# Kernel optimization log

Hardware: AMD Instinct MI355X
Metric: run time of the kernel (lower is better)

The kernel has to match this reference:

```python
import jax, jax.numpy as jnp
import numpy as np

EPS = 1e-5

def conv1x1(x, W, b):
    # x: [B,C,H,W], W: [O,C], b: [O]
    return jnp.einsum('bchw,oc->bohw', x, W) + b[None, :, None, None]

def bn_eval(x, gamma, beta, mean, var):
    inv = jax.lax.rsqrt(var + EPS)
    return (x - mean[None, :, None, None]) * (gamma * inv)[None, :, None, None] + beta[None, :, None, None]

def setup_inputs() -> dict:
    key = jax.random.key(0)
    ks = jax.random.split(key, 12)
    B, C, O = 32, 256, 256
    Hz, Wz, Hx, Wx = 7, 7, 31, 31
    s = 0.02
    inp = {
        'zf': jax.random.normal(ks[0], (B, C, Hz, Wz), jnp.float32),
        'xf': jax.random.normal(ks[1], (B, C, Hx, Wx), jnp.float32),
        'Wq': jax.random.normal(ks[2], (C, C), jnp.float32) * s,
        'bq': jnp.zeros((C,), jnp.float32),
        'Ws': jax.random.normal(ks[3], (C, C), jnp.float32) * s,
        'bs': jnp.zeros((C,), jnp.float32),
        'Wg': jax.random.normal(ks[4], (C, C), jnp.float32) * s,
        'bg': jnp.zeros((C,), jnp.float32),
        'g_gamma': jnp.ones((C,), jnp.float32),
        'g_beta': jnp.zeros((C,), jnp.float32),
        'g_mean': jnp.zeros((C,), jnp.float32),
        'g_var': jnp.ones((C,), jnp.float32),
        'Wfi': jax.random.normal(ks[5], (O, 3 * C), jnp.float32) * s,
        'bfi': jnp.zeros((O,), jnp.float32),
        'fi_gamma': jnp.ones((O,), jnp.float32),
        'fi_beta': jnp.zeros((O,), jnp.float32),
        'fi_mean': jnp.zeros((O,), jnp.float32),
        'fi_var': jnp.ones((O,), jnp.float32),
    }
    return inp

def reference(zf, xf, Wq, bq, Ws, bs, Wg, bg, g_gamma, g_beta, g_mean, g_var,
              Wfi, bfi, fi_gamma, fi_beta, fi_mean, fi_var):
    B, C, Hx, Wx = xf.shape
    _, _, Hz, Wz = zf.shape
    Nx, Nz = Hx * Wx, Hz * Wz

    xf_trans = conv1x1(xf, Wq, bq)                 # [B,C,Hx,Wx]
    zf_trans = conv1x1(zf, Ws, bs)                 # [B,C,Hz,Wz]
    xf_g = jax.nn.relu(bn_eval(conv1x1(xf, Wg, bg), g_gamma, g_beta, g_mean, g_var))
    zf_g = jax.nn.relu(bn_eval(conv1x1(zf, Wg, bg), g_gamma, g_beta, g_mean, g_var))

    zf_g_p = zf_g.reshape(B, C, Nz).transpose(0, 2, 1)      # [B,Nz,C]
    xf_g_p = xf_g.reshape(B, C, Nx).transpose(0, 2, 1)      # [B,Nx,C]
    zf_t = zf_trans.reshape(B, C, Nz)                        # [B,C,Nz]
    xf_t_q = xf_trans.reshape(B, C, Nx).transpose(0, 2, 1)  # [B,Nx,C]
    xf_t_k = xf_trans.reshape(B, C, Nx)                      # [B,C,Nx]

    similar = jax.nn.softmax(jnp.einsum('bnc,bcm->bnm', xf_t_q, zf_t), axis=2)      # [B,Nx,Nz]
    self_similar = jax.nn.softmax(jnp.einsum('bnc,bcm->bnm', xf_t_q, xf_t_k), axis=2)  # [B,Nx,Nx]

    self_emb = jnp.einsum('bnm,bmc->bnc', self_similar, xf_g_p).transpose(0, 2, 1).reshape(B, C, Hx, Wx)
    emb = jnp.einsum('bnm,bmc->bnc', similar, zf_g_p).transpose(0, 2, 1).reshape(B, C, Hx, Wx)

    out = jnp.concatenate([emb, self_emb, xf_g], axis=1)     # [B,3C,Hx,Wx]
    out = jax.nn.relu(bn_eval(conv1x1(out, Wfi, bfi), fi_gamma, fi_beta, fi_mean, fi_var))
    return out
```

## Files before the change

kernel.cpp:

```cpp
#include <hip/hip_runtime.h>
#include <hip/hip_bf16.h>

#define EPS 1e-5f

constexpr int B    = 32;
constexpr int C    = 256;
constexpr int O    = 256;
constexpr int NZ   = 49;
constexpr int NX   = 961;
constexpr int NXP  = 1024;
constexpr int NZP  = 128;
constexpr int C3   = 768;

typedef short  bf16x8 __attribute__((ext_vector_type(8)));
typedef float  f32x4  __attribute__((ext_vector_type(4)));

#define AS1 __attribute__((address_space(1)))
#define AS3 __attribute__((address_space(3)))

__device__ inline ushort f2bf(float f) {
    union { float f; uint u; } v; v.f = f;
    uint r = v.u + 0x7fffu + ((v.u >> 16) & 1u);
    return (ushort)(r >> 16);
}

template<int ACT, bool BIAS_COL, bool OUT_BF16>
__global__ __launch_bounds__(256)
void mfma_nt(const ushort* __restrict__ Abase, long sA, int lda,
             const ushort* __restrict__ Bbase, long sB, int ldb,
             void* __restrict__ Cbase, long sC, int ldc, int Nstore,
             int K,
             const float* __restrict__ bias,
             const float* __restrict__ gamma, const float* __restrict__ beta,
             const float* __restrict__ mean,  const float* __restrict__ varr)
{
    __shared__ ushort As[4096];
    __shared__ ushort Bs[4096];

    const int b   = blockIdx.z;
    const ushort* A  = Abase + (long)b * sA;
    const ushort* Bm = Bbase + (long)b * sB;
    const int i0 = blockIdx.y * 128;
    const int j0 = blockIdx.x * 128;

    const int tid  = threadIdx.x;
    const int lane = tid & 63;
    const int wid  = tid >> 6;
    const int wrow = wid >> 1, wcol = wid & 1;

    const int s0 = wid * 128 + lane;
    const int s1 = s0 + 64;
    auto soff = [](int s, int ld) {
        int row = s >> 2;
        int kq  = (s & 3) ^ ((s >> 3) & 3);
        return (long)row * ld + kq * 8;
    };
    const ushort* gA0 = A  + (long)i0 * lda + soff(s0, lda);
    const ushort* gA1 = A  + (long)i0 * lda + soff(s1, lda);
    const ushort* gB0 = Bm + (long)j0 * ldb + soff(s0, ldb);
    const ushort* gB1 = Bm + (long)j0 * ldb + soff(s1, ldb);

    ushort* lA0 = As + wid * 1024;
    ushort* lA1 = As + wid * 1024 + 512;
    ushort* lB0 = Bs + wid * 1024;
    ushort* lB1 = Bs + wid * 1024 + 512;

    const int rl = lane & 15, kq = lane >> 4;
    int aoff[4], boff[4];
    #pragma unroll
    for (int f = 0; f < 4; ++f) {
        int ra = wrow * 64 + f * 16 + rl;
        int ba = (ra * 64 + kq * 16) ^ ((ra & 6) << 3);
        aoff[f] = ba >> 1;
        int rb = wcol * 64 + f * 16 + rl;
        int bb = (rb * 64 + kq * 16) ^ ((rb & 6) << 3);
        boff[f] = bb >> 1;
    }

    f32x4 acc[4][4];
    #pragma unroll
    for (int i = 0; i < 4; ++i)
        #pragma unroll
        for (int j = 0; j < 4; ++j)
            acc[i][j] = (f32x4){0.f, 0.f, 0.f, 0.f};

    for (int k0 = 0; k0 < K; k0 += 32) {
        __builtin_amdgcn_global_load_lds((const AS1 void*)gA0, (AS3 void*)lA0, 16, 0, 0);
        __builtin_amdgcn_global_load_lds((const AS1 void*)gA1, (AS3 void*)lA1, 16, 0, 0);
        __builtin_amdgcn_global_load_lds((const AS1 void*)gB0, (AS3 void*)lB0, 16, 0, 0);
        __builtin_amdgcn_global_load_lds((const AS1 void*)gB1, (AS3 void*)lB1, 16, 0, 0);
        gA0 += 32; gA1 += 32; gB0 += 32; gB1 += 32;
        __syncthreads();

        bf16x8 av[4], bv[4];
        #pragma unroll
        for (int f = 0; f < 4; ++f) av[f] = *(const bf16x8*)(As + aoff[f]);
        #pragma unroll
        for (int f = 0; f < 4; ++f) bv[f] = *(const bf16x8*)(Bs + boff[f]);

        #pragma unroll
        for (int i = 0; i < 4; ++i)
            #pragma unroll
            for (int j = 0; j < 4; ++j)
                acc[i][j] = __builtin_amdgcn_mfma_f32_16x16x32_bf16(av[i], bv[j], acc[i][j], 0, 0, 0);
        __syncthreads();
    }

    const int jb = j0 + wcol * 64 + rl;
    const int ib = i0 + wrow * 64 + kq * 4;

    ushort* Cb16 = (ushort*)Cbase + (long)b * sC;
    float*  Cb32 = (float*)Cbase + (long)b * sC;

    #pragma unroll
    for (int fj = 0; fj < 4; ++fj) {
        int gj = jb + fj * 16;
        if (gj >= Nstore) continue;
        float sc = 1.f, sh = 0.f;
        if (ACT >= 1 && BIAS_COL) {
            float add = bias[gj];
            if (ACT == 2) {
                float inv = rsqrtf(varr[gj] + EPS);
                sc = gamma[gj] * inv;
                sh = (add - mean[gj]) * sc + beta[gj];
            } else {
                sh = add;
            }
        }
        #pragma unroll
        for (int fi = 0; fi < 4; ++fi) {
            #pragma unroll
            for (int r = 0; r < 4; ++r) {
                int gi = ib + fi * 16 + r;
                float v = acc[fi][fj][r];
                if (ACT >= 1) {
                    if (BIAS_COL) {
                        v = v * sc + sh;
                        if (ACT == 2) v = fmaxf(v, 0.f);
                    } else {
                        float add = bias[gi];
                        if (ACT == 2) {
                            float inv = rsqrtf(varr[gi] + EPS);
                            float s2 = gamma[gi] * inv;
                            v = v * s2 + (add - mean[gi]) * s2 + beta[gi];
                            v = fmaxf(v, 0.f);
                        } else {
                            v += add;
                        }
                    }
                }
                long off = (long)gi * ldc + gj;
                if (OUT_BF16) Cb16[off] = f2bf(v);
                else          Cb32[off] = v;
            }
        }
    }
}

template<int KVPAD, int VALID, int LDV>
__global__ __launch_bounds__(256)
void flash_attn(const ushort* __restrict__ Qm,
                const ushort* __restrict__ Km, long sK,
                const ushort* __restrict__ Vm,
                ushort* __restrict__ Outm)
{
    __shared__ ushort Ks[64 * 256];
    __shared__ ushort Vs[256 * 64];
    __shared__ ushort plds[4][1024];

    int wg = blockIdx.x;
    wg = (wg & 7) * 64 + (wg >> 3);
    const int b  = wg >> 4;
    const int qt = wg & 15;

    const int tid  = threadIdx.x;
    const int wid  = tid >> 6;
    const int lane = tid & 63;
    const int rl   = lane & 15;
    const int g    = lane >> 4;

    const ushort* Qp = Qm + (long)b * NXP * C + (long)(qt * 64 + wid * 16 + rl) * C + g * 8;
    bf16x8 aq[8];
    #pragma unroll
    for (int ks = 0; ks < 8; ++ks) aq[ks] = *(const bf16x8*)(Qp + ks * 32);

    const ushort* Kb = Km + (long)b * sK;
    const ushort* Vb = Vm + (long)b * C * LDV;

    int offK[8], offV[8];
    #pragma unroll
    for (int i = 0; i < 8; ++i) {
        int s = i * 256 + tid;
        int row = s >> 5, kq = s & 31;
        offK[i] = row * C + ((kq ^ (row & 7)) * 8);
        int c = s >> 3, mk = s & 7;
        offV[i] = c * LDV + ((mk ^ (c & 7)) * 8);
    }

    f32x4 o[16];
    #pragma unroll
    for (int cs = 0; cs < 16; ++cs) o[cs] = (f32x4){0.f, 0.f, 0.f, 0.f};
    f32x4 m4 = {-3.0e38f, -3.0e38f, -3.0e38f, -3.0e38f};
    f32x4 l4 = {0.f, 0.f, 0.f, 0.f};

    ushort* pw = &plds[wid][0];
    const int swz = (rl & 7);

    for (int kv0 = 0; kv0 < KVPAD; kv0 += 64) {
        const ushort* Kt = Kb + (long)kv0 * C;
        const ushort* Vt = Vb + kv0;
        #pragma unroll
        for (int i = 0; i < 8; ++i)
            __builtin_amdgcn_global_load_lds((const AS1 void*)(Kt + offK[i]),
                                             (AS3 void*)(Ks + (i * 256 + wid * 64) * 8), 16, 0, 0);
        #pragma unroll
        for (int i = 0; i < 8; ++i)
            __builtin_amdgcn_global_load_lds((const AS1 void*)(Vt + offV[i]),
                                             (AS3 void*)(Vs + (i * 256 + wid * 64) * 8), 16, 0, 0);
        __syncthreads();

        f32x4 s[4];
        #pragma unroll
        for (int mt = 0; mt < 4; ++mt) s[mt] = (f32x4){0.f, 0.f, 0.f, 0.f};
        #pragma unroll
        for (int mt = 0; mt < 4; ++mt) {
            const ushort* krow = Ks + (mt * 16 + rl) * 256;
            #pragma unroll
            for (int ks = 0; ks < 8; ++ks) {
                const ushort* kp = krow + (((g + ks * 4) ^ swz) * 8);
                s[mt] = __builtin_amdgcn_mfma_f32_16x16x32_bf16(aq[ks], *(const bf16x8*)kp, s[mt], 0, 0, 0);
            }
        }

        if (kv0 + 64 > VALID) {
            #pragma unroll
            for (int mt = 0; mt < 4; ++mt)
                if (kv0 + mt * 16 + rl >= VALID)
                    s[mt] = (f32x4){-3.0e38f, -3.0e38f, -3.0e38f, -3.0e38f};
        }

        f32x4 pm;
        #pragma unroll
        for (int r = 0; r < 4; ++r)
            pm[r] = fmaxf(fmaxf(s[0][r], s[1][r]), fmaxf(s[2][r], s[3][r]));
        #pragma unroll
        for (int r = 0; r < 4; ++r) {
            float v = pm[r];
            v = fmaxf(v, __shfl_xor(v, 1));
            v = fmaxf(v, __shfl_xor(v, 2));
            v = fmaxf(v, __shfl_xor(v, 4));
            v = fmaxf(v, __shfl_xor(v, 8));
            pm[r] = v;
        }

        f32x4 sc;
        #pragma unroll
        for (int r = 0; r < 4; ++r) {
            float mn = fmaxf(m4[r], pm[r]);
            sc[r] = __expf(m4[r] - mn);
            m4[r] = mn;
        }

        #pragma unroll
        for (int mt = 0; mt < 4; ++mt)
            #pragma unroll
            for (int r = 0; r < 4; ++r)
                s[mt][r] = __expf(s[mt][r] - m4[r]);

        f32x4 rs;
        #pragma unroll
        for (int r = 0; r < 4; ++r)
            rs[r] = (s[0][r] + s[1][r]) + (s[2][r] + s[3][r]);
        #pragma unroll
        for (int r = 0; r < 4; ++r) {
            float v = rs[r];
            v += __shfl_xor(v, 1);
            v += __shfl_xor(v, 2);
            v += __shfl_xor(v, 4);
            v += __shfl_xor(v, 8);
            rs[r] = v;
        }
        #pragma unroll
        for (int r = 0; r < 4; ++r) l4[r] = l4[r] * sc[r] + rs[r];

        #pragma unroll
        for (int cs = 0; cs < 16; ++cs)
            #pragma unroll
            for (int r = 0; r < 4; ++r)
                o[cs][r] *= sc[r];

        #pragma unroll
        for (int mt = 0; mt < 4; ++mt)
            #pragma unroll
            for (int r = 0; r < 4; ++r) {
                int row = g * 4 + r;
                int idx = (row * 64 + mt * 16 + rl) ^ ((row & 7) << 3);
                pw[idx] = f2bf(s[mt][r]);
            }

        bf16x8 pa[2];
        #pragma unroll
        for (int ks2 = 0; ks2 < 2; ++ks2) {
            int idx = (rl * 64 + ks2 * 32 + g * 8) ^ ((rl & 7) << 3);
            pa[ks2] = *(const bf16x8*)(pw + idx);
        }

        #pragma unroll
        for (int cs = 0; cs < 16; ++cs) {
            const ushort* vrow = Vs + (cs * 16 + rl) * 64;
            const ushort* vp0 = vrow + ((g ^ swz) * 8);
            const ushort* vp1 = vrow + (((g + 4) ^ swz) * 8);
            o[cs] = __builtin_amdgcn_mfma_f32_16x16x32_bf16(pa[0], *(const bf16x8*)vp0, o[cs], 0, 0, 0);
            o[cs] = __builtin_amdgcn_mfma_f32_16x16x32_bf16(pa[1], *(const bf16x8*)vp1, o[cs], 0, 0, 0);
        }
        __syncthreads();
    }

    f32x4 inv;
    #pragma unroll
    for (int r = 0; r < 4; ++r) inv[r] = 1.0f / l4[r];

    ushort* ob = Outm + (long)b * NXP * C3 + (long)(qt * 64 + wid * 16) * C3;
    #pragma unroll
    for (int cs = 0; cs < 16; ++cs)
        #pragma unroll
        for (int r = 0; r < 4; ++r)
            ob[(long)(g * 4 + r) * C3 + cs * 16 + rl] = f2bf(o[cs][r] * inv[r]);
}

__global__ __launch_bounds__(256)
void transpose_cvt(const float* __restrict__ src, ushort* __restrict__ dst,
                   int Cc, int Nsrc, int Npad)
{
    const int bz = blockIdx.z;
    src += (long)bz * Cc * Nsrc;
    dst += (long)bz * Npad * Cc;
    const int c0 = blockIdx.x * 32, n0 = blockIdx.y * 32;
    __shared__ float t[32][33];
    const int lx = threadIdx.x & 31, ly = threadIdx.x >> 5;
    #pragma unroll
    for (int r = 0; r < 32; r += 8) {
        int n = n0 + lx;
        t[ly + r][lx] = (n < Nsrc) ? src[(long)(c0 + ly + r) * Nsrc + n] : 0.f;
    }
    __syncthreads();
    #pragma unroll
    for (int r = 0; r < 32; r += 8) {
        int n = n0 + ly + r;
        if (n < Npad) dst[(long)n * Cc + c0 + lx] = f2bf(t[lx][ly + r]);
    }
}

__global__ void cvt_bf(const float* __restrict__ src, ushort* __restrict__ dst, int n)
{
    int i = blockIdx.x * 256 + threadIdx.x;
    if (i < n) dst[i] = f2bf(src[i]);
}

extern "C" void kernel_launch(void* const* d_in, const int* in_sizes, int n_in,
                              void* d_out, int out_size, void* d_ws, size_t ws_size,
                              hipStream_t stream)
{
    const float* zf       = (const float*)d_in[0];
    const float* xf       = (const float*)d_in[1];
    const float* Wq       = (const float*)d_in[2];
    const float* bq       = (const float*)d_in[3];
    const float* Ws       = (const float*)d_in[4];
    const float* bs       = (const float*)d_in[5];
    const float* Wg       = (const float*)d_in[6];
    const float* bg       = (const float*)d_in[7];
    const float* g_gamma  = (const float*)d_in[8];
    const float* g_beta   = (const float*)d_in[9];
    const float* g_mean   = (const float*)d_in[10];
    const float* g_var    = (const float*)d_in[11];
    const float* Wfi      = (const float*)d_in[12];
    const float* bfi      = (const float*)d_in[13];
    const float* fi_gamma = (const float*)d_in[14];
    const float* fi_beta  = (const float*)d_in[15];
    const float* fi_mean  = (const float*)d_in[16];
    const float* fi_var   = (const float*)d_in[17];
    float* out = (float*)d_out;

    char* w = (char*)d_ws;
    auto alloc = [&](long bytes) { char* p = w; w += (bytes + 255) & ~255L; return p; };
    ushort* xfT     = (ushort*)alloc(2L * B * NXP * C);
    ushort* xqT     = (ushort*)alloc(2L * B * NXP * C);
    ushort* concatT = (ushort*)alloc(2L * B * NXP * C3);
    ushort* gate_cn = (ushort*)alloc(2L * B * C * NXP);
    ushort* zfT     = (ushort*)alloc(2L * B * NZP * C);
    ushort* zsT     = (ushort*)alloc(2L * B * NZP * C);
    ushort* zg_cn   = (ushort*)alloc(2L * B * C * NZP);
    ushort* Wq_bf   = (ushort*)alloc(2L * C * C);
    ushort* Ws_bf   = (ushort*)alloc(2L * C * C);
    ushort* Wg_bf   = (ushort*)alloc(2L * C * C);
    ushort* Wfi_bf  = (ushort*)alloc(2L * O * C3);

    cvt_bf<<<dim3((C * C + 255) / 256), 256, 0, stream>>>(Wq, Wq_bf, C * C);
    cvt_bf<<<dim3((C * C + 255) / 256), 256, 0, stream>>>(Ws, Ws_bf, C * C);
    cvt_bf<<<dim3((C * C + 255) / 256), 256, 0, stream>>>(Wg, Wg_bf, C * C);
    cvt_bf<<<dim3((O * C3 + 255) / 256), 256, 0, stream>>>(Wfi, Wfi_bf, O * C3);
    transpose_cvt<<<dim3(C / 32, NXP / 32, B), 256, 0, stream>>>(xf, xfT, C, NX, NXP);
    transpose_cvt<<<dim3(C / 32, NZP / 32, B), 256, 0, stream>>>(zf, zfT, C, NZ, NZP);

    mfma_nt<1, true, true><<<dim3(2, 8, B), 256, 0, stream>>>(
        xfT, (long)NXP * C, C, Wq_bf, 0, C,
        xqT, (long)NXP * C, C, C, C, bq, nullptr, nullptr, nullptr, nullptr);

    mfma_nt<2, true, true><<<dim3(2, 8, B), 256, 0, stream>>>(
        xfT, (long)NXP * C, C, Wg_bf, 0, C,
        concatT + 2 * C, (long)NXP * C3, C3, C, C, bg, g_gamma, g_beta, g_mean, g_var);

    mfma_nt<2, false, true><<<dim3(8, 2, B), 256, 0, stream>>>(
        Wg_bf, 0, C, xfT, (long)NXP * C, C,
        gate_cn, (long)C * NXP, NXP, NXP, C, bg, g_gamma, g_beta, g_mean, g_var);

    mfma_nt<1, true, true><<<dim3(2, 1, B), 256, 0, stream>>>(
        zfT, (long)NZP * C, C, Ws_bf, 0, C,
        zsT, (long)NZP * C, C, C, C, bs, nullptr, nullptr, nullptr, nullptr);

    mfma_nt<2, false, true><<<dim3(1, 2, B), 256, 0, stream>>>(
        Wg_bf, 0, C, zfT, (long)NZP * C, C,
        zg_cn, (long)C * NZP, NZP, NZP, C, bg, g_gamma, g_beta, g_mean, g_var);

    flash_attn<64, NZ, NZP><<<dim3(512), 256, 0, stream>>>(
        xqT, zsT, (long)NZP * C, zg_cn, concatT);

    flash_attn<NXP, NX, NXP><<<dim3(512), 256, 0, stream>>>(
        xqT, xqT, (long)NXP * C, gate_cn, concatT + C);

    mfma_nt<2, false, false><<<dim3(8, 2, B), 256, 0, stream>>>(
        Wfi_bf, 0, C3, concatT, (long)NXP * C3, C3,
        out, (long)O * NX, NX, NX, C3, bfi, fi_gamma, fi_beta, fi_mean, fi_var);
}
```

Before: 341.1 us.

## Register-prefetch smaller KV tiles with lazy softmax rescale in flash attention

Shrinks the flash-attention KV tile from 64 to 32 rows and replaces the direct global-to-LDS loads with a register prefetch of the next tile, issued after the barrier so the loads overlap the current tile's MFMA work. Adds a lazy online-softmax rescale that only updates the running max, sum and output when some row's max grows by more than 8. Trims the self-attention KV loop to 992 to skip the all-padding final tile. The smaller LDS footprint may raise occupancy, but halving the tile doubles the barriers per row block and the lazy threshold lets exp values grow up to e^8 before rescaling.

```diff
diff --git a/kernel.cpp b/kernel.cpp
--- a/kernel.cpp
+++ b/kernel.cpp
@@ -164,9 +164,10 @@
                 const ushort* __restrict__ Vm,
                 ushort* __restrict__ Outm)
 {
-    __shared__ ushort Ks[64 * 256];
-    __shared__ ushort Vs[256 * 64];
-    __shared__ ushort plds[4][1024];
+    constexpr int NT = KVPAD / 32;
+    __shared__ ushort Ks[32 * 256];
+    __shared__ ushort Vs[256 * 32];
+    __shared__ ushort plds[4][512];
 
     int wg = blockIdx.x;
     wg = (wg & 7) * 64 + (wg >> 3);
@@ -187,14 +188,16 @@
     const ushort* Kb = Km + (long)b * sK;
     const ushort* Vb = Vm + (long)b * C * LDV;
 
-    int offK[8], offV[8];
-    #pragma unroll
-    for (int i = 0; i < 8; ++i) {
-        int s = i * 256 + tid;
-        int row = s >> 5, kq = s & 31;
-        offK[i] = row * C + ((kq ^ (row & 7)) * 8);
-        int c = s >> 3, mk = s & 7;
-        offV[i] = c * LDV + ((mk ^ (c & 7)) * 8);
+    int offKg[4], offKl[4], offVg[4], offVl[4];
+    #pragma unroll
+    for (int i = 0; i < 4; ++i) {
+        int ck = i * 256 + tid;
+        int krow = ck >> 5, kq = ck & 31;
+        offKg[i] = krow * C + kq * 8;
+        offKl[i] = (krow * 32 + (kq ^ (krow & 7))) * 8;
+        int vrow = ck >> 2, mk = ck & 3;
+        offVg[i] = vrow * LDV + mk * 8;
+        offVl[i] = (vrow * 4 + (mk ^ (vrow & 3))) * 8;
     }
 
     f32x4 o[16];
@@ -204,45 +207,54 @@
     f32x4 l4 = {0.f, 0.f, 0.f, 0.f};
 
     ushort* pw = &plds[wid][0];
-    const int swz = (rl & 7);
-
-    for (int kv0 = 0; kv0 < KVPAD; kv0 += 64) {
-        const ushort* Kt = Kb + (long)kv0 * C;
-        const ushort* Vt = Vb + kv0;
-        #pragma unroll
-        for (int i = 0; i < 8; ++i)
-            __builtin_amdgcn_global_load_lds((const AS1 void*)(Kt + offK[i]),
-                                             (AS3 void*)(Ks + (i * 256 + wid * 64) * 8), 16, 0, 0);
-        #pragma unroll
-        for (int i = 0; i < 8; ++i)
-            __builtin_amdgcn_global_load_lds((const AS1 void*)(Vt + offV[i]),
-                                             (AS3 void*)(Vs + (i * 256 + wid * 64) * 8), 16, 0, 0);
+
+    bf16x8 kreg[4], vreg[4];
+    #pragma unroll
+    for (int i = 0; i < 4; ++i) kreg[i] = *(const bf16x8*)(Kb + offKg[i]);
+    #pragma unroll
+    for (int i = 0; i < 4; ++i) vreg[i] = *(const bf16x8*)(Vb + offVg[i]);
+
+    for (int t = 0; t < NT; ++t) {
+        #pragma unroll
+        for (int i = 0; i < 4; ++i) *(bf16x8*)(Ks + offKl[i]) = kreg[i];
+        #pragma unroll
+        for (int i = 0; i < 4; ++i) *(bf16x8*)(Vs + offVl[i]) = vreg[i];
         __syncthreads();
 
-        f32x4 s[4];
-        #pragma unroll
-        for (int mt = 0; mt < 4; ++mt) s[mt] = (f32x4){0.f, 0.f, 0.f, 0.f};
-        #pragma unroll
-        for (int mt = 0; mt < 4; ++mt) {
-            const ushort* krow = Ks + (mt * 16 + rl) * 256;
+        if (t + 1 < NT) {
+            const ushort* Kt = Kb + (long)(t + 1) * 32 * C;
+            const ushort* Vt = Vb + (t + 1) * 32;
+            #pragma unroll
+            for (int i = 0; i < 4; ++i) kreg[i] = *(const bf16x8*)(Kt + offKg[i]);
+            #pragma unroll
+            for (int i = 0; i < 4; ++i) vreg[i] = *(const bf16x8*)(Vt + offVg[i]);
+        }
+
+        const int kv0 = t * 32;
+
+        f32x4 s[2];
+        s[0] = (f32x4){0.f, 0.f, 0.f, 0.f};
+        s[1] = (f32x4){0.f, 0.f, 0.f, 0.f};
+        #pragma unroll
+        for (int mt = 0; mt < 2; ++mt) {
+            const ushort* krow_p = Ks + (mt * 16 + rl) * 256;
             #pragma unroll
             for (int ks = 0; ks < 8; ++ks) {
-                const ushort* kp = krow + (((g + ks * 4) ^ swz) * 8);
+                const ushort* kp = krow_p + (((ks * 4 + g) ^ (rl & 7)) * 8);
                 s[mt] = __builtin_amdgcn_mfma_f32_16x16x32_bf16(aq[ks], *(const bf16x8*)kp, s[mt], 0, 0, 0);
             }
         }
 
-        if (kv0 + 64 > VALID) {
-            #pragma unroll
-            for (int mt = 0; mt < 4; ++mt)
+        if (kv0 + 32 > VALID) {
+            #pragma unroll
+            for (int mt = 0; mt < 2; ++mt)
                 if (kv0 + mt * 16 + rl >= VALID)
                     s[mt] = (f32x4){-3.0e38f, -3.0e38f, -3.0e38f, -3.0e38f};
         }
 
         f32x4 pm;
         #pragma unroll
-        for (int r = 0; r < 4; ++r)
-            pm[r] = fmaxf(fmaxf(s[0][r], s[1][r]), fmaxf(s[2][r], s[3][r]));
+        for (int r = 0; r < 4; ++r) pm[r] = fmaxf(s[0][r], s[1][r]);
         #pragma unroll
         for (int r = 0; r < 4; ++r) {
             float v = pm[r];
@@ -253,24 +265,33 @@
             pm[r] = v;
         }
 
-        f32x4 sc;
-        #pragma unroll
-        for (int r = 0; r < 4; ++r) {
-            float mn = fmaxf(m4[r], pm[r]);
-            sc[r] = __expf(m4[r] - mn);
-            m4[r] = mn;
-        }
-
-        #pragma unroll
-        for (int mt = 0; mt < 4; ++mt)
+        int ok = (pm[0] <= m4[0] + 8.f) && (pm[1] <= m4[1] + 8.f) &&
+                 (pm[2] <= m4[2] + 8.f) && (pm[3] <= m4[3] + 8.f);
+        if (!__all(ok)) {
+            f32x4 sc;
+            #pragma unroll
+            for (int r = 0; r < 4; ++r) {
+                float mn = fmaxf(m4[r], pm[r]);
+                sc[r] = __expf(m4[r] - mn);
+                m4[r] = mn;
+            }
+            #pragma unroll
+            for (int r = 0; r < 4; ++r) l4[r] *= sc[r];
+            #pragma unroll
+            for (int cs = 0; cs < 16; ++cs)
+                #pragma unroll
+                for (int r = 0; r < 4; ++r) o[cs][r] *= sc[r];
+        }
+
+        #pragma unroll
+        for (int mt = 0; mt < 2; ++mt)
             #pragma unroll
             for (int r = 0; r < 4; ++r)
                 s[mt][r] = __expf(s[mt][r] - m4[r]);
 
         f32x4 rs;
         #pragma unroll
-        for (int r = 0; r < 4; ++r)
-            rs[r] = (s[0][r] + s[1][r]) + (s[2][r] + s[3][r]);
+        for (int r = 0; r < 4; ++r) rs[r] = s[0][r] + s[1][r];
         #pragma unroll
         for (int r = 0; r < 4; ++r) {
             float v = rs[r];
@@ -278,40 +299,26 @@
             v += __shfl_xor(v, 2);
             v += __shfl_xor(v, 4);
             v += __shfl_xor(v, 8);
-            rs[r] = v;
-        }
-        #pragma unroll
-        for (int r = 0; r < 4; ++r) l4[r] = l4[r] * sc[r] + rs[r];
-
-        #pragma unroll
-        for (int cs = 0; cs < 16; ++cs)
-            #pragma unroll
-            for (int r = 0; r < 4; ++r)
-                o[cs][r] *= sc[r];
-
-        #pragma unroll
-        for (int mt = 0; mt < 4; ++mt)
+            l4[r] += v;
+        }
+
+        #pragma unroll
+        for (int mt = 0; mt < 2; ++mt)
             #pragma unroll
             for (int r = 0; r < 4; ++r) {
                 int row = g * 4 + r;
-                int idx = (row * 64 + mt * 16 + rl) ^ ((row & 7) << 3);
+                int chunk = mt * 2 + (rl >> 3);
+                int idx = row * 32 + ((chunk ^ (row >> 2)) * 8) + (rl & 7);
                 pw[idx] = f2bf(s[mt][r]);
             }
 
-        bf16x8 pa[2];
-        #pragma unroll
-        for (int ks2 = 0; ks2 < 2; ++ks2) {
-            int idx = (rl * 64 + ks2 * 32 + g * 8) ^ ((rl & 7) << 3);
-            pa[ks2] = *(const bf16x8*)(pw + idx);
-        }
+        bf16x8 pa = *(const bf16x8*)(pw + rl * 32 + ((g ^ (rl >> 2)) * 8));
 
         #pragma unroll
         for (int cs = 0; cs < 16; ++cs) {
-            const ushort* vrow = Vs + (cs * 16 + rl) * 64;
-            const ushort* vp0 = vrow + ((g ^ swz) * 8);
-            const ushort* vp1 = vrow + (((g + 4) ^ swz) * 8);
-            o[cs] = __builtin_amdgcn_mfma_f32_16x16x32_bf16(pa[0], *(const bf16x8*)vp0, o[cs], 0, 0, 0);
-            o[cs] = __builtin_amdgcn_mfma_f32_16x16x32_bf16(pa[1], *(const bf16x8*)vp1, o[cs], 0, 0, 0);
+            int c = cs * 16 + rl;
+            const ushort* vp = Vs + c * 32 + ((g ^ (c & 3)) * 8);
+            o[cs] = __builtin_amdgcn_mfma_f32_16x16x32_bf16(pa, *(const bf16x8*)vp, o[cs], 0, 0, 0);
         }
         __syncthreads();
     }
@@ -425,7 +432,7 @@
     flash_attn<64, NZ, NZP><<<dim3(512), 256, 0, stream>>>(
         xqT, zsT, (long)NZP * C, zg_cn, concatT);
 
-    flash_attn<NXP, NX, NXP><<<dim3(512), 256, 0, stream>>>(
+    flash_attn<992, NX, NXP><<<dim3(512), 256, 0, stream>>>(
         xqT, xqT, (long)NXP * C, gate_cn, concatT + C);
 
     mfma_nt<2, false, false><<<dim3(8, 2, B), 256, 0, stream>>>(
```

After: 332.0 us. -2.7%, faster.
